# Kernel optimization log

Measured on AMD Instinct MI355X. Metric: run time of the kernel, lower is better.

The kernel has to match this reference:

```python
import jax, jax.numpy as jnp
import numpy as np

# dims matching input_specs / init_kwargs
S_BATCH, T_BATCH, NUM, DIM, H, W = 4, 4, 8, 512, 32, 32
K = 64              # self.k, number of kmeans clusters
KMEANS_ITERS = 10   # fixed Lloyd iterations (stand-in for kmeans-to-convergence)


def _kmeans(points):
    """Euclidean Lloyd kmeans. points: [n, d] -> centers [K, d].
    Deterministic init: first K points. Empty clusters keep old center."""
    centers0 = points[:K]
    sq_p = jnp.sum(points * points, axis=1)  # [n]

    def step(centers, _):
        # squared euclidean distance [n, K]
        d2 = sq_p[:, None] + jnp.sum(centers * centers, axis=1)[None, :] \
             - 2.0 * points @ centers.T
        assign = jnp.argmin(d2, axis=1)                      # [n]
        onehot = jax.nn.one_hot(assign, K, dtype=points.dtype)  # [n, K]
        counts = onehot.sum(axis=0)                          # [K]
        sums = onehot.T @ points                             # [K, d]
        new = jnp.where(counts[:, None] > 0,
                        sums / jnp.maximum(counts, 1.0)[:, None],
                        centers)
        return new, None

    centers, _ = jax.lax.scan(step, centers0, None, length=KMEANS_ITERS)
    return centers


def setup_inputs() -> dict:
    key = jax.random.key(0)
    k1, k2, k3, k4 = jax.random.split(key, 4)
    return {
        "source_feat": jax.random.normal(k1, (S_BATCH, NUM, DIM, H, W), dtype=jnp.float32),
        "target_feat": jax.random.normal(k2, (T_BATCH, NUM, DIM, H, W), dtype=jnp.float32),
        "source_label": jax.random.randint(k3, (S_BATCH,), 0, 10),
        "target_label": jax.random.randint(k4, (T_BATCH,), 0, 10),
    }


def reference(source_feat, target_feat, source_label, target_label):
    sb, num, dim, h, w = source_feat.shape
    tb = target_feat.shape[0]

    # view each map as (h*w, dim) point cloud, kmeans per (batch, num)
    s_pts = source_feat.reshape(sb, num, dim, h * w).transpose(0, 1, 3, 2)
    t_pts = target_feat.reshape(tb, num, dim, h * w).transpose(0, 1, 3, 2)
    km = jax.vmap(jax.vmap(_kmeans))
    cs = km(s_pts).transpose(1, 0, 2, 3)  # [num, sb, K, dim]
    ct = km(t_pts).transpose(1, 0, 2, 3)  # [num, tb, K, dim]

    # mat_dist for every (num, i, j) pair of center sets: [num, sb, tb, K, K]
    sq_s = jnp.sum(cs * cs, axis=-1)  # [num, sb, K]
    sq_t = jnp.sum(ct * ct, axis=-1)  # [num, tb, K]
    dots = jnp.einsum('nikd,njld->nijkl', cs, ct)
    dist = jnp.sqrt(jnp.maximum(
        sq_s[:, :, None, :, None] + sq_t[:, None, :, None, :] - 2.0 * dots, 0.0))
    y = jnp.argmin(dist, axis=-1)  # [num, sb, tb, K] nearest target center per source center

    # gather matched target centers; replicate source centers over j (torch append order: i, j, k)
    ct_b = jnp.broadcast_to(ct[:, None], (num, sb, tb, K, dim))
    t_mat = jnp.take_along_axis(ct_b, y[..., None], axis=3)            # [num, sb, tb, K, dim]
    s_mat = jnp.broadcast_to(cs[:, :, None], (num, sb, tb, K, dim))

    N = sb * tb * K
    s_mat = s_mat.reshape(num, N, dim)
    t_mat = t_mat.reshape(num, N, dim)

    # trans_mat[k] = s_mat.T @ pinv(t_mat.T)   -> [num, dim, dim]
    pinv_t = jnp.linalg.pinv(t_mat.transpose(0, 2, 1))  # pinv([dim, N]) -> [num, N, dim]
    trans_mat = jnp.einsum('nkd,nke->nde', s_mat, pinv_t)
    return trans_mat
```

## Files before the change

### kernel.cpp

```cpp
#include <hip/hip_runtime.h>

typedef unsigned int u32;
typedef unsigned long long u64;

#define NPTS  1024
#define DIMD  512
#define KCL   64
#define KMIT  10

constexpr size_t O_CTG  = 0;
constexpr size_t O_SUMS = O_CTG  + 64ull*512*64;
constexpr size_t O_CNT  = O_SUMS + 64ull*64*512;
constexpr size_t O_SQC  = O_CNT  + 64ull*64;
constexpr size_t O_SQP  = O_SQC  + 64ull*64;
constexpr size_t O_ASG  = O_SQP  + 64ull*1024;
constexpr size_t O_CTN  = O_ASG  + 64ull*1024;
constexpr size_t O_Y    = O_CTN  + 8ull*256*512;
constexpr size_t O_CNT2 = O_Y    + 8ull*4*4*64;
constexpr size_t O_BM   = O_CNT2 + 8ull*256;
constexpr size_t O_G    = O_BM   + 8ull*256*512;
constexpr size_t O_LT   = O_G    + 8ull*256*256;
constexpr size_t O_YB   = O_LT   + 8ull*256*256;
constexpr size_t O_ZB   = O_YB   + 8ull*256*512;
constexpr size_t O_PTST = O_ZB   + 8ull*256*512;

constexpr size_t O_PS0 = O_SUMS;
constexpr size_t O_PS1 = O_CTN;
static_assert(O_PS1 + 64ull*64*512 <= O_G, "PS1 overlay must fit before O_G");

constexpr size_t O_BEST = O_G;

constexpr size_t O_CS = O_SUMS;
constexpr size_t O_W  = O_YB;
constexpr size_t O_WT = O_YB + 8ull*4*64*64;

__device__ __forceinline__ const float* run_base(const float* s, const float* t, int run){
    const float* b = (run < 32) ? s : t;
    return b + (size_t)(run & 31) * (DIMD * NPTS);
}
__device__ __forceinline__ u64 dpack(float d2, int c){
    u32 u = __float_as_uint(d2);
    u = (u & 0x80000000u) ? ~u : (u | 0x80000000u);
    return ((u64)u << 32) | (u32)c;
}
__device__ __forceinline__ float rdlane(float v, int l){
    return __uint_as_float(__builtin_amdgcn_readlane(__float_as_uint(v), l));
}

__global__ __launch_bounds__(256) void k_init(const float* __restrict__ src, const float* __restrict__ tgt,
                                              float* __restrict__ ws){
    int bx = blockIdx.x; int run = bx >> 2, q = bx & 3;
    int tid = threadIdx.x;
    const float* base = run_base(src, tgt, run);
    int p = q*256 + tid;
    float acc = 0.f;
    for (int d = 0; d < DIMD; ++d){
        float v = base[(size_t)d*NPTS + p];
        acc = fmaf(v, v, acc);
    }
    ws[O_SQP + run*NPTS + p] = acc;
    if (q == 0){
        if (tid < KCL) ws[O_SQC + run*KCL + tid] = acc;
        if (tid < KCL) ((int*)(ws + O_CNT))[run*KCL + tid] = 0;
        for (int idx = tid; idx < DIMD*KCL; idx += 256){
            int d = idx >> 6, c = idx & 63;
            ws[O_CTG + (size_t)run*DIMD*KCL + idx] = base[(size_t)d*NPTS + c];
        }
    }
}

__global__ __launch_bounds__(256) void k_ptsT(const float* __restrict__ src, const float* __restrict__ tgt,
                                              float* __restrict__ ws){
    int bx = blockIdx.x; int dt = bx & 7, pt = (bx >> 3) & 15, run = bx >> 7;
    int tid = threadIdx.x, lane = tid & 63, r4 = tid >> 6;
    const float* base = run_base(src, tgt, run);
    __shared__ float t[64*65];
    for (int pass = 0; pass < 16; ++pass){
        int r = pass*4 + r4;
        t[r*65 + lane] = base[(size_t)(dt*64 + r)*NPTS + pt*64 + lane];
    }
    __syncthreads();
    for (int pass = 0; pass < 16; ++pass){
        int p = pass*4 + r4;
        ws[O_PTST + ((size_t)run*NPTS + pt*64 + p)*DIMD + dt*64 + lane] = t[lane*65 + p];
    }
}

__global__ __launch_bounds__(256, 4) void k_assign(const float* __restrict__ src, const float* __restrict__ tgt,
                                                   const float* __restrict__ ctr, const float* __restrict__ sqc,
                                                   const float* __restrict__ sqp,
                                                   u64* __restrict__ bestg){
    int bxx = blockIdx.x;
    int cb  = (bxx >> 3) & 1;
    int w   = ((bxx >> 4) << 3) | (bxx & 7);
    int run = w >> 3, qt = w & 7;
    int tid = threadIdx.x, lane = tid & 63;
    int g = __builtin_amdgcn_readfirstlane(tid >> 6);
    int c0 = cb*32 + g*8;
    const float* base = run_base(src, tgt, run);
    const float* cg = ctr + (size_t)run*DIMD*KCL + c0;
    int p0 = qt*128 + 2*lane;
    float acc[2][8] = {};
    __shared__ u64 red[4][128];

#define LOADP(P, DB) { \
    _Pragma("unroll") \
    for (int u = 0; u < 8; ++u) \
        P[u] = *(const float2*)&base[(size_t)((DB)*8 + u)*NPTS + p0]; }

#define COMPUTE(P, DB) { \
    _Pragma("unroll") \
    for (int u = 0; u < 8; ++u){ \
        const float4* cp = (const float4*)(cg + (size_t)((DB)*8 + u)*KCL); \
        float4 c0v = cp[0], c1v = cp[1]; \
        float cv[8] = {c0v.x,c0v.y,c0v.z,c0v.w, c1v.x,c1v.y,c1v.z,c1v.w}; \
        _Pragma("unroll") \
        for (int cl = 0; cl < 8; ++cl){ \
            acc[0][cl] = fmaf(P[u].x, cv[cl], acc[0][cl]); \
            acc[1][cl] = fmaf(P[u].y, cv[cl], acc[1][cl]); \
        } \
    } }

    float2 pa[8], pb[8];
    LOADP(pa, 0);
    for (int db = 0; db < 64; db += 2){
        if (db + 1 < 64) LOADP(pb, db + 1);
        COMPUTE(pa, db);
        if (db + 2 < 64) LOADP(pa, db + 2);
        COMPUTE(pb, db + 1);
    }
#undef LOADP
#undef COMPUTE

    const float* sqcg = sqc + run*KCL + c0;
    float sq[8];
    #pragma unroll
    for (int q = 0; q < 8; ++q) sq[q] = sqcg[q];
    float2 sq2 = *(const float2*)&sqp[run*NPTS + p0];
    #pragma unroll
    for (int s = 0; s < 2; ++s){
        float sqpv = s ? sq2.y : sq2.x;
        u64 best = dpack(sqpv + sq[0] - 2.f*acc[s][0], c0);
        #pragma unroll
        for (int cl = 1; cl < 8; ++cl){
            u64 k2 = dpack(sqpv + sq[cl] - 2.f*acc[s][cl], c0 + cl);
            best = (k2 < best) ? k2 : best;
        }
        red[g][2*lane + s] = best;
    }
    __syncthreads();
    if (tid < 128){
        u64 b = red[0][tid];
        #pragma unroll
        for (int g2 = 1; g2 < 4; ++g2){ u64 k2 = red[g2][tid]; b = (k2 < b) ? k2 : b; }
        bestg[(((size_t)(run*8 + qt)*128 + tid) << 1) + cb] = b;
    }
}

__global__ __launch_bounds__(256) void k_sums(float* __restrict__ ws){
    int bx = blockIdx.x; int pg = bx & 1, dh = (bx >> 1) & 1, run = bx >> 2;
    int tid = threadIdx.x;
    __shared__ float sm[KCL*256];
    __shared__ int a[512];
    const u64* bestg = (const u64*)(ws + O_BEST);
    int* cnt = (int*)(ws + O_CNT);
    for (int idx = tid; idx < 512; idx += 256){
        int p = pg*512 + idx;
        int qt = p >> 7, t = p & 127;
        const u64* bp = bestg + (((size_t)(run*8 + qt)*128 + t) << 1);
        u64 x = bp[0], y = bp[1];
        u64 m = (y < x) ? y : x;
        int c = (int)(m & 0xffffffffu);
        a[idx] = c;
        if (dh == 0) atomicAdd(&cnt[run*KCL + c], 1);
    }
    for (int idx = tid; idx < KCL*256; idx += 256) sm[idx] = 0.f;
    __syncthreads();
    const float* pT = ws + O_PTST + ((size_t)run*NPTS + pg*512)*DIMD + dh*256 + tid;
    for (int p = 0; p < 512; p += 4){
        float v0 = pT[(size_t)(p+0)*DIMD], v1 = pT[(size_t)(p+1)*DIMD];
        float v2 = pT[(size_t)(p+2)*DIMD], v3 = pT[(size_t)(p+3)*DIMD];
        sm[a[p+0]*256 + tid] += v0;
        sm[a[p+1]*256 + tid] += v1;
        sm[a[p+2]*256 + tid] += v2;
        sm[a[p+3]*256 + tid] += v3;
    }
    __syncthreads();
    size_t psx = pg ? O_PS1 : O_PS0;
    for (int c = 0; c < KCL; ++c)
        ws[psx + ((size_t)run*KCL + c)*DIMD + dh*256 + tid] = sm[c*256 + tid];
}

__global__ __launch_bounds__(256) void k_newc(float* __restrict__ ws){
    int run = blockIdx.x, tid = threadIdx.x;
    __shared__ float sm2[KCL*65];
    __shared__ int cl[KCL];
    int* cnt = (int*)(ws + O_CNT);
    if (tid < KCL) cl[tid] = cnt[run*KCL + tid];
    __syncthreads();
    if (tid < KCL) cnt[run*KCL + tid] = 0;
    float sqa = 0.f;
    for (int dc = 0; dc < 8; ++dc){
        for (int idx = tid; idx < KCL*64; idx += 256){
            int c = idx >> 6, dl = idx & 63;
            size_t o = ((size_t)run*KCL + c)*DIMD + dc*64 + dl;
            sm2[c*65 + dl] = ws[O_PS0 + o] + ws[O_PS1 + o];
        }
        __syncthreads();
        for (int idx = tid; idx < KCL*64; idx += 256){
            int dl = idx >> 6, c = idx & 63, d = dc*64 + dl;
            size_t gi = O_CTG + (size_t)run*DIMD*KCL + d*KCL + c;
            float old = ws[gi];
            int cc = cl[c];
            float nv = (cc > 0) ? sm2[c*65 + dl] / (float)cc : old;
            ws[gi] = nv;
            sm2[c*65 + dl] = nv;
        }
        __syncthreads();
        if (tid < KCL){
            for (int dl = 0; dl < 64; ++dl){ float v = sm2[tid*65 + dl]; sqa = fmaf(v, v, sqa); }
        }
        __syncthreads();
    }
    if (tid < KCL) ws[O_SQC + run*KCL + tid] = sqa;
}

__global__ __launch_bounds__(256) void k_ctn(float* __restrict__ ws){
    int bx = blockIdx.x; int dc = bx & 7, jj = (bx >> 3) & 3, n = (bx >> 5) & 7, st = bx >> 8;
    int run = st ? (jj*8 + n) : (32 + jj*8 + n);
    int tid = threadIdx.x, lane = tid & 63, r4 = tid >> 6;
    __shared__ float t[64*65];
    for (int pass = 0; pass < 16; ++pass){
        int r = pass*4 + r4;
        t[r*65 + lane] = ws[O_CTG + (size_t)run*DIMD*KCL + (dc*64 + r)*KCL + lane];
    }
    __syncthreads();
    size_t dstbase = st ? (O_CS  + ((size_t)(n*4 + jj)*64)*DIMD)
                        : (O_CTN + ((size_t)n*256 + jj*64)*DIMD);
    for (int pass = 0; pass < 16; ++pass){
        int l = pass*4 + r4;
        ws[dstbase + (size_t)l*DIMD + dc*64 + lane] = t[lane*65 + l];
    }
}

__global__ __launch_bounds__(256) void k_map(float* __restrict__ ws){
    int bx = blockIdx.x; int j = bx & 3, i = (bx >> 2) & 3, n = bx >> 4;
    int run_s = i*8 + n, run_t = 32 + j*8 + n;
    int tid = threadIdx.x, lane = tid & 63;
    int g = __builtin_amdgcn_readfirstlane(tid >> 6);
    const float* cgs = ws + O_CTG + (size_t)run_s*DIMD*KCL + lane;
    const float* cgt = ws + O_CTG + (size_t)run_t*DIMD*KCL + g*16;
    float acc[16] = {};
    for (int d = 0; d < DIMD; ++d){
        float csv = cgs[d*KCL];
        const float4* cp = (const float4*)(cgt + d*KCL);
        float4 c0=cp[0], c1=cp[1], c2=cp[2], c3=cp[3];
        float cv[16] = {c0.x,c0.y,c0.z,c0.w, c1.x,c1.y,c1.z,c1.w,
                        c2.x,c2.y,c2.z,c2.w, c3.x,c3.y,c3.z,c3.w};
        #pragma unroll
        for (int cl = 0; cl < 16; ++cl) acc[cl] = fmaf(csv, cv[cl], acc[cl]);
    }
    float sqs = ws[O_SQC + run_s*KCL + lane];
    const float* sqtp = ws + O_SQC + run_t*KCL + g*16;
    u64 best = dpack(sqs + sqtp[0] - 2.f*acc[0], g*16);
    #pragma unroll
    for (int cl = 1; cl < 16; ++cl){
        u64 k2 = dpack(sqs + sqtp[cl] - 2.f*acc[cl], g*16 + cl);
        best = (k2 < best) ? k2 : best;
    }
    __shared__ u64 red[4][64];
    red[g][lane] = best;
    __syncthreads();
    if (tid < 64){
        u64 b = red[0][tid];
        #pragma unroll
        for (int g2 = 1; g2 < 4; ++g2){ u64 k2 = red[g2][tid]; b = (k2 < b) ? k2 : b; }
        int l = (int)(b & 0xffffffffu);
        int* yv   = (int*)(ws + O_Y);
        int* cnt2 = (int*)(ws + O_CNT2);
        yv[((n*4 + i)*4 + j)*64 + tid] = l;
        atomicAdd(&cnt2[n*256 + j*64 + l], 1);
    }
}

__global__ __launch_bounds__(256) void k_bmat(float* __restrict__ ws){
    int bx = blockIdx.x; int dh = bx & 1, j = (bx >> 1) & 3, n = bx >> 3;
    int tid = threadIdx.x;
    __shared__ float Bacc[KCL*256];
    __shared__ int yl[256];
    __shared__ int c2[KCL];
    const int* yv   = (const int*)(ws + O_Y);
    const int* cnt2 = (const int*)(ws + O_CNT2);
    { int i = tid >> 6, k = tid & 63; yl[tid] = yv[((n*4 + i)*4 + j)*64 + k]; }
    if (tid < KCL) c2[tid] = cnt2[n*256 + j*64 + tid];
    for (int idx = tid; idx < KCL*256; idx += 256) Bacc[idx] = 0.f;
    __syncthreads();
    const float* cs = ws + O_CS + (size_t)(n*4)*64*DIMD + dh*256 + tid;
    #pragma unroll 4
    for (int s = 0; s < 256; ++s){
        int l = yl[s];
        float v = cs[(size_t)s*DIMD];
        Bacc[l*256 + tid] += v;
    }
    __syncthreads();
    for (int l = 0; l < KCL; ++l){
        int cc = c2[l]; if (cc < 1) cc = 1;
        ws[O_BM + ((size_t)n*256 + j*64 + l)*DIMD + dh*256 + tid] = Bacc[l*256 + tid] / (float)cc;
    }
}

__global__ __launch_bounds__(256) void k_gram(float* __restrict__ ws){
    int bx = blockIdx.x; int cc = bx & 7, n = bx >> 3;
    int tid = threadIdx.x, llane = tid & 63, jlane = tid >> 6;
    int run_t = 32 + jlane*8 + n;
    const float* bbase = ws + O_CTG + (size_t)run_t*DIMD*KCL + llane;
    const float* arow  = ws + O_CTN + (size_t)(n*256 + cc*32)*DIMD;
    float acc[32] = {};
    for (int d = 0; d < DIMD; d += 4){
        float bv0 = bbase[(d+0)*KCL], bv1 = bbase[(d+1)*KCL];
        float bv2 = bbase[(d+2)*KCL], bv3 = bbase[(d+3)*KCL];
        #pragma unroll
        for (int c = 0; c < 32; ++c){
            const float4 av = *(const float4*)&arow[c*DIMD + d];
            acc[c] = fmaf(av.x, bv0, acc[c]);
            acc[c] = fmaf(av.y, bv1, acc[c]);
            acc[c] = fmaf(av.z, bv2, acc[c]);
            acc[c] = fmaf(av.w, bv3, acc[c]);
        }
    }
    const int* cnt2 = (const int*)(ws + O_CNT2);
    bool used_cp = cnt2[n*256 + tid] > 0;
    float* Gp = ws + O_G + (size_t)n*65536;
    #pragma unroll
    for (int c = 0; c < 32; ++c){
        int cg = cc*32 + c;
        bool used_c = cnt2[n*256 + cg] > 0;
        float v = (used_c && used_cp) ? acc[c] : ((cg == tid) ? 1.f : 0.f);
        Gp[(size_t)cg*256 + tid] = v;
    }
}

__global__ __launch_bounds__(256, 1) void k_chol(float* __restrict__ ws){
    int n = blockIdx.x, tid = threadIdx.x;
    int lane = tid & 63, wv = tid >> 6;
    float* Gn  = ws + O_G  + (size_t)n*65536;
    float* LTn = ws + O_LT + (size_t)n*65536;
    __shared__ __align__(16) float Pc[64*200];

    for (int kb = 0; kb < 4; ++kb){
        int c0 = kb*64, r1 = c0 + 64, rem = 256 - r1;
        float dreg[64];
        {
            const float* grow = Gn + (size_t)(c0+lane)*256 + c0;
            #pragma unroll
            for (int j4 = 0; j4 < 16; ++j4){
                float4 v = *(const float4*)&grow[j4*4];
                dreg[j4*4+0]=v.x; dreg[j4*4+1]=v.y; dreg[j4*4+2]=v.z; dreg[j4*4+3]=v.w;
            }
        }
        float preg[64];
        int prow = (wv-1)*64 + lane;
        bool pact = (wv >= 1) && (prow < rem);
        {
            const float* growp = Gn + (size_t)(r1+prow)*256 + c0;
            #pragma unroll
            for (int j4 = 0; j4 < 16; ++j4){
                if (pact){
                    float4 v = *(const float4*)&growp[j4*4];
                    preg[j4*4+0]=v.x; preg[j4*4+1]=v.y; preg[j4*4+2]=v.z; preg[j4*4+3]=v.w;
                } else {
                    preg[j4*4+0]=0.f; preg[j4*4+1]=0.f; preg[j4*4+2]=0.f; preg[j4*4+3]=0.f;
                }
            }
        }
        #pragma unroll
        for (int k = 0; k < 64; ++k){
            float dkk = sqrtf(fmaxf(rdlane(dreg[k], k), 1e-30f));
            float inv = 1.f / dkk;
            dreg[k] = (lane == k) ? dkk : dreg[k]*inv;
            preg[k] *= inv;
            #pragma unroll
            for (int j = k+1; j < 64; ++j){
                float s = rdlane(dreg[k], j);
                dreg[j] = fmaf(-dreg[k], s, dreg[j]);
                preg[j] = fmaf(-preg[k], s, preg[j]);
            }
        }
        if (wv == 0){
            float* grow = Gn + (size_t)(c0+lane)*256 + c0;
            #pragma unroll
            for (int j4 = 0; j4 < 16; ++j4){
                float4 v; v.x=dreg[j4*4+0]; v.y=dreg[j4*4+1]; v.z=dreg[j4*4+2]; v.w=dreg[j4*4+3];
                *(float4*)&grow[j4*4] = v;
            }
        }
        if (pact){
            float* growp = Gn + (size_t)(r1+prow)*256 + c0;
            #pragma unroll
            for (int j4 = 0; j4 < 16; ++j4){
                float4 v; v.x=preg[j4*4+0]; v.y=preg[j4*4+1]; v.z=preg[j4*4+2]; v.w=preg[j4*4+3];
                *(float4*)&growp[j4*4] = v;
            }
            float* ltp = LTn + (size_t)c0*256 + r1 + prow;
            #pragma unroll
            for (int j = 0; j < 64; ++j) ltp[(size_t)j*256] = preg[j];
            #pragma unroll
            for (int j = 0; j < 64; ++j) Pc[j*200 + prow] = preg[j];
        }
        __syncthreads();
        if (rem > 0){
            int nt4 = rem >> 2;
            int ntiles = nt4*(nt4+1)/2;
            for (int t = tid; t < ntiles; t += 256){
                int ti = (int)((sqrtf(8.f*(float)t + 1.f) - 1.f) * 0.5f);
                while ((ti+1)*(ti+2)/2 <= t) ++ti;
                while (ti*(ti+1)/2 > t) --ti;
                int tj = t - ti*(ti+1)/2;
                int i0 = ti*4, j0 = tj*4;
                float acc[4][4] = {};
                for (int k = 0; k < 64; ++k){
                    const float4 pi = *(const float4*)&Pc[k*200 + i0];
                    const float4 pj = *(const float4*)&Pc[k*200 + j0];
                    float pir[4] = {pi.x,pi.y,pi.z,pi.w};
                    float pjr[4] = {pj.x,pj.y,pj.z,pj.w};
                    #pragma unroll
                    for (int r = 0; r < 4; ++r)
                        #pragma unroll
                        for (int s = 0; s < 4; ++s)
                            acc[r][s] = fmaf(pir[r], pjr[s], acc[r][s]);
                }
                #pragma unroll
                for (int r = 0; r < 4; ++r){
                    float* grow = Gn + (size_t)(r1+i0+r)*256 + r1 + j0;
                    #pragma unroll
                    for (int s = 0; s < 4; ++s) grow[s] -= acc[r][s];
                }
            }
        }
        __syncthreads();
    }
}

__global__ __launch_bounds__(256, 1) void k_dinv(float* __restrict__ ws){
    int n = blockIdx.x, tid = threadIdx.x;
    int lane = tid & 63, kb = tid >> 6;
    const float* Gn = ws + O_G + (size_t)n*65536;
    __shared__ __align__(16) float DlT[4][64*65];
    for (int idx = lane; idx < 1024; idx += 64){
        int r = idx >> 4, c4 = idx & 15;
        float4 v = *(const float4*)&Gn[(size_t)(kb*64 + r)*256 + kb*64 + c4*4];
        DlT[kb][(c4*4+0)*65 + r] = v.x;
        DlT[kb][(c4*4+1)*65 + r] = v.y;
        DlT[kb][(c4*4+2)*65 + r] = v.z;
        DlT[kb][(c4*4+3)*65 + r] = v.w;
    }
    __syncthreads();
    float x[64];
    #pragma unroll
    for (int i = 0; i < 64; ++i) x[i] = (i == lane) ? 1.f : 0.f;
    const float* Dk = DlT[kb];
    #pragma unroll
    for (int k = 0; k < 64; ++k){
        float invd = 1.f / Dk[k*65 + k];
        x[k] *= invd;
        #pragma unroll
        for (int i = k+1; i < 64; ++i)
            x[i] = fmaf(-Dk[k*65 + i], x[k], x[i]);
    }
    float* Wg  = ws + O_W  + ((size_t)n*4 + kb)*4096;
    float* WTg = ws + O_WT + ((size_t)n*4 + kb)*4096;
    #pragma unroll
    for (int r = 0; r < 64; ++r) Wg[r*64 + lane] = x[r];
    #pragma unroll
    for (int r4 = 0; r4 < 16; ++r4){
        float4 v; v.x=x[r4*4+0]; v.y=x[r4*4+1]; v.z=x[r4*4+2]; v.w=x[r4*4+3];
        *(float4*)&WTg[lane*64 + r4*4] = v;
    }
}

__global__ __launch_bounds__(256, 1) void k_solve(float* __restrict__ ws){
    int n = blockIdx.x, cg = blockIdx.y;
    int tid = threadIdx.x;
    int tx = tid & 15, ty = tid >> 4;
    const float* Gn  = ws + O_G  + (size_t)n*65536;
    const float* LTn = ws + O_LT + (size_t)n*65536;
    const float* Ct  = ws + O_CTN + (size_t)n*256*DIMD + (size_t)cg*64;
    const float* Wg  = ws + O_W  + (size_t)n*4*4096;
    const float* WTg = ws + O_WT + (size_t)n*4*4096;
    float* Zb = ws + O_ZB + (size_t)n*256*DIMD + (size_t)cg*64;

    __shared__ __align__(16) float YL[4][64*65];
    __shared__ __align__(16) float At[64*65];
    __shared__ __align__(16) float RL[64*65];

    float acc[4][4];
    for (int bi = 0; bi < 4; ++bi){
        #pragma unroll
        for (int a = 0; a < 4; ++a){
            float4 v = *(const float4*)&Ct[(size_t)(bi*64 + ty*4 + a)*DIMD + tx*4];
            acc[a][0]=v.x; acc[a][1]=v.y; acc[a][2]=v.z; acc[a][3]=v.w;
        }
        for (int j = 0; j < bi; ++j){
            __syncthreads();
            for (int idx = tid; idx < 1024; idx += 256){
                int k = idx >> 4, r4 = idx & 15;
                float4 v = *(const float4*)&LTn[(size_t)(j*64 + k)*256 + bi*64 + r4*4];
                *(float4*)&At[k*65 + r4*4] = v;
            }
            __syncthreads();
            const float* Yj = YL[j];
            #pragma unroll 8
            for (int k = 0; k < 64; ++k){
                float4 av = *(const float4*)&At[k*65 + ty*4];
                float4 yv = *(const float4*)&Yj[k*65 + tx*4];
                float ar[4] = {av.x,av.y,av.z,av.w};
                float yr[4] = {yv.x,yv.y,yv.z,yv.w};
                #pragma unroll
                for (int a = 0; a < 4; ++a)
                    #pragma unroll
                    for (int b = 0; b < 4; ++b)
                        acc[a][b] = fmaf(-ar[a], yr[b], acc[a][b]);
            }
        }
        __syncthreads();
        #pragma unroll
        for (int a = 0; a < 4; ++a){
            float4 v; v.x=acc[a][0]; v.y=acc[a][1]; v.z=acc[a][2]; v.w=acc[a][3];
            *(float4*)&RL[(ty*4 + a)*65 + tx*4] = v;
        }
        for (int idx = tid; idx < 1024; idx += 256){
            int k = idx >> 4, r4 = idx & 15;
            float4 v = *(const float4*)&WTg[(size_t)bi*4096 + k*64 + r4*4];
            *(float4*)&At[k*65 + r4*4] = v;
        }
        __syncthreads();
        float out[4][4] = {};
        #pragma unroll 8
        for (int k = 0; k < 64; ++k){
            float4 av = *(const float4*)&At[k*65 + ty*4];
            float4 rv = *(const float4*)&RL[k*65 + tx*4];
            float ar[4] = {av.x,av.y,av.z,av.w};
            float rr[4] = {rv.x,rv.y,rv.z,rv.w};
            #pragma unroll
            for (int a = 0; a < 4; ++a)
                #pragma unroll
                for (int b = 0; b < 4; ++b)
                    out[a][b] = fmaf(ar[a], rr[b], out[a][b]);
        }
        float* Yi = YL[bi];
        #pragma unroll
        for (int a = 0; a < 4; ++a){
            float4 v; v.x=out[a][0]; v.y=out[a][1]; v.z=out[a][2]; v.w=out[a][3];
            *(float4*)&Yi[(ty*4 + a)*65 + tx*4] = v;
        }
    }
    for (int bi = 3; bi >= 0; --bi){
        __syncthreads();
        #pragma unroll
        for (int a = 0; a < 4; ++a){
            float4 v = *(const float4*)&YL[bi][(ty*4 + a)*65 + tx*4];
            acc[a][0]=v.x; acc[a][1]=v.y; acc[a][2]=v.z; acc[a][3]=v.w;
        }
        for (int j = bi+1; j < 4; ++j){
            __syncthreads();
            for (int idx = tid; idx < 1024; idx += 256){
                int k = idx >> 4, r4 = idx & 15;
                float4 v = *(const float4*)&Gn[(size_t)(j*64 + k)*256 + bi*64 + r4*4];
                *(float4*)&At[k*65 + r4*4] = v;
            }
            __syncthreads();
            const float* Zj = YL[j];
            #pragma unroll 8
            for (int k = 0; k < 64; ++k){
                float4 av = *(const float4*)&At[k*65 + ty*4];
                float4 zv = *(const float4*)&Zj[k*65 + tx*4];
                float ar[4] = {av.x,av.y,av.z,av.w};
                float zr[4] = {zv.x,zv.y,zv.z,zv.w};
                #pragma unroll
                for (int a = 0; a < 4; ++a)
                    #pragma unroll
                    for (int b = 0; b < 4; ++b)
                        acc[a][b] = fmaf(-ar[a], zr[b], acc[a][b]);
            }
        }
        __syncthreads();
        #pragma unroll
        for (int a = 0; a < 4; ++a){
            float4 v; v.x=acc[a][0]; v.y=acc[a][1]; v.z=acc[a][2]; v.w=acc[a][3];
            *(float4*)&RL[(ty*4 + a)*65 + tx*4] = v;
        }
        for (int idx = tid; idx < 1024; idx += 256){
            int k = idx >> 4, r4 = idx & 15;
            float4 v = *(const float4*)&Wg[(size_t)bi*4096 + k*64 + r4*4];
            *(float4*)&At[k*65 + r4*4] = v;
        }
        __syncthreads();
        float out[4][4] = {};
        #pragma unroll 8
        for (int k = 0; k < 64; ++k){
            float4 av = *(const float4*)&At[k*65 + ty*4];
            float4 rv = *(const float4*)&RL[k*65 + tx*4];
            float ar[4] = {av.x,av.y,av.z,av.w};
            float rr[4] = {rv.x,rv.y,rv.z,rv.w};
            #pragma unroll
            for (int a = 0; a < 4; ++a)
                #pragma unroll
                for (int b = 0; b < 4; ++b)
                    out[a][b] = fmaf(ar[a], rr[b], out[a][b]);
        }
        float* Zi = YL[bi];
        #pragma unroll
        for (int a = 0; a < 4; ++a){
            float4 v; v.x=out[a][0]; v.y=out[a][1]; v.z=out[a][2]; v.w=out[a][3];
            *(float4*)&Zi[(ty*4 + a)*65 + tx*4] = v;
            *(float4*)&Zb[(size_t)(bi*64 + ty*4 + a)*DIMD + tx*4] = v;
        }
    }
}

__global__ __launch_bounds__(256) void k_gemmE(const float* __restrict__ ws, float* __restrict__ out){
    int bx = blockIdx.x; int et = bx & 7, dt = (bx >> 3) & 7, n = bx >> 6;
    int tid = threadIdx.x;
    __shared__ float Bl[256*64];
    __shared__ float Zl[256*64];
    const float* Bm = ws + O_BM + (size_t)n*256*DIMD;
    const float* Zb = ws + O_ZB + (size_t)n*256*DIMD;
    for (int idx = tid; idx < 16384; idx += 256){
        int c = idx >> 6, dd = idx & 63;
        Bl[idx] = Bm[(size_t)c*DIMD + dt*64 + dd];
        Zl[idx] = Zb[(size_t)c*DIMD + et*64 + dd];
    }
    __syncthreads();
    int td = tid & 15, te = tid >> 4;
    float acc[4][4] = {};
    for (int c = 0; c < 256; ++c){
        float4 bv = *(const float4*)&Bl[c*64 + td*4];
        float4 zv = *(const float4*)&Zl[c*64 + te*4];
        float b4[4] = {bv.x, bv.y, bv.z, bv.w};
        float z4[4] = {zv.x, zv.y, zv.z, zv.w};
        #pragma unroll
        for (int r = 0; r < 4; ++r)
            #pragma unroll
            for (int s = 0; s < 4; ++s) acc[r][s] = fmaf(b4[r], z4[s], acc[r][s]);
    }
    float* ob = out + (size_t)n*262144 + (size_t)(dt*64 + td*4)*DIMD + et*64 + te*4;
    #pragma unroll
    for (int r = 0; r < 4; ++r){
        float4 o; o.x = acc[r][0]; o.y = acc[r][1]; o.z = acc[r][2]; o.w = acc[r][3];
        *(float4*)&ob[(size_t)r*DIMD] = o;
    }
}

extern "C" void kernel_launch(void* const* d_in, const int* in_sizes, int n_in,
                              void* d_out, int out_size, void* d_ws, size_t ws_size,
                              hipStream_t stream){
    const float* src = (const float*)d_in[0];
    const float* tgt = (const float*)d_in[1];
    float* ws  = (float*)d_ws;
    float* out = (float*)d_out;

    k_init<<<256, 256, 0, stream>>>(src, tgt, ws);
    k_ptsT<<<8192, 256, 0, stream>>>(src, tgt, ws);

    for (int it = 0; it < KMIT; ++it){
        k_assign<<<1024, 256, 0, stream>>>(src, tgt,
                                           ws + O_CTG, ws + O_SQC, ws + O_SQP,
                                           (u64*)(ws + O_BEST));
        k_sums<<<256, 256, 0, stream>>>(ws);
        k_newc<<<64, 256, 0, stream>>>(ws);
    }

    hipMemsetAsync((char*)d_ws + O_CNT2*4, 0, 8*256*4, stream);
    k_ctn<<<512, 256, 0, stream>>>(ws);
    k_map<<<128, 256, 0, stream>>>(ws);
    k_bmat<<<64, 256, 0, stream>>>(ws);
    k_gram<<<64, 256, 0, stream>>>(ws);
    k_chol<<<8, 256, 0, stream>>>(ws);
    k_dinv<<<8, 256, 0, stream>>>(ws);
    k_solve<<<dim3(8, 8), 256, 0, stream>>>(ws);
    k_gemmE<<<512, 256, 0, stream>>>(ws, out);
}
```

Measured before the change: 2.413 ms.

## Split blocked Cholesky into panel and trailing-update kernels; deepen assign prefetch

The single-block-per-matrix Cholesky is split into a per-panel factor kernel and a separate trailing-update kernel launched across 64 blocks per step. The trailing update now reads the panel from global memory instead of shared memory. The aim is to spread the serial Cholesky work across many more CUs, at the cost of extra launches and global reads. Separately, the k_assign loop now loads and computes 16 dimensions per stage instead of 8, which raises register pressure.

```diff
diff --git a/kernel.cpp b/kernel.cpp
--- a/kernel.cpp
+++ b/kernel.cpp
@@ -103,15 +103,15 @@
     float acc[2][8] = {};
     __shared__ u64 red[4][128];
 
-#define LOADP(P, DB) { \
+#define LOADP(P, B) { \
     _Pragma("unroll") \
-    for (int u = 0; u < 8; ++u) \
-        P[u] = *(const float2*)&base[(size_t)((DB)*8 + u)*NPTS + p0]; }
-
-#define COMPUTE(P, DB) { \
+    for (int u = 0; u < 16; ++u) \
+        P[u] = *(const float2*)&base[(size_t)((B)*16 + u)*NPTS + p0]; }
+
+#define COMPUTE(P, B) { \
     _Pragma("unroll") \
-    for (int u = 0; u < 8; ++u){ \
-        const float4* cp = (const float4*)(cg + (size_t)((DB)*8 + u)*KCL); \
+    for (int u = 0; u < 16; ++u){ \
+        const float4* cp = (const float4*)(cg + (size_t)((B)*16 + u)*KCL); \
         float4 c0v = cp[0], c1v = cp[1]; \
         float cv[8] = {c0v.x,c0v.y,c0v.z,c0v.w, c1v.x,c1v.y,c1v.z,c1v.w}; \
         _Pragma("unroll") \
@@ -121,13 +121,13 @@
         } \
     } }
 
-    float2 pa[8], pb[8];
+    float2 pa[16], pb[16];
     LOADP(pa, 0);
-    for (int db = 0; db < 64; db += 2){
-        if (db + 1 < 64) LOADP(pb, db + 1);
-        COMPUTE(pa, db);
-        if (db + 2 < 64) LOADP(pa, db + 2);
-        COMPUTE(pb, db + 1);
+    for (int b = 0; b < 32; b += 2){
+        if (b + 1 < 32) LOADP(pb, b + 1);
+        COMPUTE(pa, b);
+        if (b + 2 < 32) LOADP(pa, b + 2);
+        COMPUTE(pb, b + 1);
     }
 #undef LOADP
 #undef COMPUTE
@@ -340,104 +340,115 @@
     }
 }
 
-__global__ __launch_bounds__(256, 1) void k_chol(float* __restrict__ ws){
+__global__ __launch_bounds__(256, 1) void k_cholp(float* __restrict__ ws, int kb){
     int n = blockIdx.x, tid = threadIdx.x;
     int lane = tid & 63, wv = tid >> 6;
     float* Gn  = ws + O_G  + (size_t)n*65536;
     float* LTn = ws + O_LT + (size_t)n*65536;
-    __shared__ __align__(16) float Pc[64*200];
-
-    for (int kb = 0; kb < 4; ++kb){
-        int c0 = kb*64, r1 = c0 + 64, rem = 256 - r1;
-        float dreg[64];
-        {
-            const float* grow = Gn + (size_t)(c0+lane)*256 + c0;
+    int c0 = kb*64, r1 = c0 + 64, rem = 256 - r1;
+
+    float dreg[64];
+    {
+        const float* grow = Gn + (size_t)(c0+lane)*256 + c0;
+        #pragma unroll
+        for (int j4 = 0; j4 < 16; ++j4){
+            float4 v = *(const float4*)&grow[j4*4];
+            dreg[j4*4+0]=v.x; dreg[j4*4+1]=v.y; dreg[j4*4+2]=v.z; dreg[j4*4+3]=v.w;
+        }
+    }
+    float preg[64];
+    int prow = (wv-1)*64 + lane;
+    bool pact = (wv >= 1) && (prow < rem);
+    {
+        const float* growp = Gn + (size_t)(r1+prow)*256 + c0;
+        #pragma unroll
+        for (int j4 = 0; j4 < 16; ++j4){
+            if (pact){
+                float4 v = *(const float4*)&growp[j4*4];
+                preg[j4*4+0]=v.x; preg[j4*4+1]=v.y; preg[j4*4+2]=v.z; preg[j4*4+3]=v.w;
+            } else {
+                preg[j4*4+0]=0.f; preg[j4*4+1]=0.f; preg[j4*4+2]=0.f; preg[j4*4+3]=0.f;
+            }
+        }
+    }
+    #pragma unroll
+    for (int k = 0; k < 64; ++k){
+        float dkk = sqrtf(fmaxf(rdlane(dreg[k], k), 1e-30f));
+        float inv = 1.f / dkk;
+        dreg[k] = (lane == k) ? dkk : dreg[k]*inv;
+        preg[k] *= inv;
+        #pragma unroll
+        for (int j = k+1; j < 64; ++j){
+            float s = rdlane(dreg[k], j);
+            dreg[j] = fmaf(-dreg[k], s, dreg[j]);
+            preg[j] = fmaf(-preg[k], s, preg[j]);
+        }
+    }
+    if (wv == 0){
+        float* grow = Gn + (size_t)(c0+lane)*256 + c0;
+        #pragma unroll
+        for (int j4 = 0; j4 < 16; ++j4){
+            float4 v; v.x=dreg[j4*4+0]; v.y=dreg[j4*4+1]; v.z=dreg[j4*4+2]; v.w=dreg[j4*4+3];
+            *(float4*)&grow[j4*4] = v;
+        }
+    }
+    if (pact){
+        float* growp = Gn + (size_t)(r1+prow)*256 + c0;
+        #pragma unroll
+        for (int j4 = 0; j4 < 16; ++j4){
+            float4 v; v.x=preg[j4*4+0]; v.y=preg[j4*4+1]; v.z=preg[j4*4+2]; v.w=preg[j4*4+3];
+            *(float4*)&growp[j4*4] = v;
+        }
+        float* ltp = LTn + (size_t)c0*256 + r1 + prow;
+        #pragma unroll
+        for (int j = 0; j < 64; ++j) ltp[(size_t)j*256] = preg[j];
+    }
+}
+
+__global__ __launch_bounds__(256) void k_trail(float* __restrict__ ws, int kb){
+    int n = blockIdx.y;
+    int c0 = kb*64, r1 = c0 + 64, rem = 256 - r1;
+    int nt4 = rem >> 2;
+    int ntiles = nt4*(nt4+1)/2;
+    float* Gn = ws + O_G + (size_t)n*65536;
+    for (int t = blockIdx.x*256 + threadIdx.x; t < ntiles; t += gridDim.x*256){
+        int ti = (int)((sqrtf(8.f*(float)t + 1.f) - 1.f) * 0.5f);
+        while ((ti+1)*(ti+2)/2 <= t) ++ti;
+        while (ti*(ti+1)/2 > t) --ti;
+        int tj = t - ti*(ti+1)/2;
+        int i0 = ti*4, j0 = tj*4;
+        const float* Li = Gn + (size_t)(r1+i0)*256 + c0;
+        const float* Lj = Gn + (size_t)(r1+j0)*256 + c0;
+        float acc[4][4] = {};
+        for (int k = 0; k < 64; k += 4){
+            float4 ar4[4], br4[4];
             #pragma unroll
-            for (int j4 = 0; j4 < 16; ++j4){
-                float4 v = *(const float4*)&grow[j4*4];
-                dreg[j4*4+0]=v.x; dreg[j4*4+1]=v.y; dreg[j4*4+2]=v.z; dreg[j4*4+3]=v.w;
+            for (int r = 0; r < 4; ++r) ar4[r] = *(const float4*)&Li[(size_t)r*256 + k];
+            #pragma unroll
+            for (int s = 0; s < 4; ++s) br4[s] = *(const float4*)&Lj[(size_t)s*256 + k];
+            #pragma unroll
+            for (int q = 0; q < 4; ++q){
+                float aq[4] = { q==0?ar4[0].x:q==1?ar4[0].y:q==2?ar4[0].z:ar4[0].w,
+                                q==0?ar4[1].x:q==1?ar4[1].y:q==2?ar4[1].z:ar4[1].w,
+                                q==0?ar4[2].x:q==1?ar4[2].y:q==2?ar4[2].z:ar4[2].w,
+                                q==0?ar4[3].x:q==1?ar4[3].y:q==2?ar4[3].z:ar4[3].w };
+                float bq[4] = { q==0?br4[0].x:q==1?br4[0].y:q==2?br4[0].z:br4[0].w,
+                                q==0?br4[1].x:q==1?br4[1].y:q==2?br4[1].z:br4[1].w,
+                                q==0?br4[2].x:q==1?br4[2].y:q==2?br4[2].z:br4[2].w,
+                                q==0?br4[3].x:q==1?br4[3].y:q==2?br4[3].z:br4[3].w };
+                #pragma unroll
+                for (int r = 0; r < 4; ++r)
+                    #pragma unroll
+                    for (int s = 0; s < 4; ++s)
+                        acc[r][s] = fmaf(aq[r], bq[s], acc[r][s]);
             }
         }
-        float preg[64];
-        int prow = (wv-1)*64 + lane;
-        bool pact = (wv >= 1) && (prow < rem);
-        {
-            const float* growp = Gn + (size_t)(r1+prow)*256 + c0;
+        #pragma unroll
+        for (int r = 0; r < 4; ++r){
+            float* grow = Gn + (size_t)(r1+i0+r)*256 + r1 + j0;
             #pragma unroll
-            for (int j4 = 0; j4 < 16; ++j4){
-                if (pact){
-                    float4 v = *(const float4*)&growp[j4*4];
-                    preg[j4*4+0]=v.x; preg[j4*4+1]=v.y; preg[j4*4+2]=v.z; preg[j4*4+3]=v.w;
-                } else {
-                    preg[j4*4+0]=0.f; preg[j4*4+1]=0.f; preg[j4*4+2]=0.f; preg[j4*4+3]=0.f;
-                }
-            }
-        }
-        #pragma unroll
-        for (int k = 0; k < 64; ++k){
-            float dkk = sqrtf(fmaxf(rdlane(dreg[k], k), 1e-30f));
-            float inv = 1.f / dkk;
-            dreg[k] = (lane == k) ? dkk : dreg[k]*inv;
-            preg[k] *= inv;
-            #pragma unroll
-            for (int j = k+1; j < 64; ++j){
-                float s = rdlane(dreg[k], j);
-                dreg[j] = fmaf(-dreg[k], s, dreg[j]);
-                preg[j] = fmaf(-preg[k], s, preg[j]);
-            }
-        }
-        if (wv == 0){
-            float* grow = Gn + (size_t)(c0+lane)*256 + c0;
-            #pragma unroll
-            for (int j4 = 0; j4 < 16; ++j4){
-                float4 v; v.x=dreg[j4*4+0]; v.y=dreg[j4*4+1]; v.z=dreg[j4*4+2]; v.w=dreg[j4*4+3];
-                *(float4*)&grow[j4*4] = v;
-            }
-        }
-        if (pact){
-            float* growp = Gn + (size_t)(r1+prow)*256 + c0;
-            #pragma unroll
-            for (int j4 = 0; j4 < 16; ++j4){
-                float4 v; v.x=preg[j4*4+0]; v.y=preg[j4*4+1]; v.z=preg[j4*4+2]; v.w=preg[j4*4+3];
-                *(float4*)&growp[j4*4] = v;
-            }
-            float* ltp = LTn + (size_t)c0*256 + r1 + prow;
-            #pragma unroll
-            for (int j = 0; j < 64; ++j) ltp[(size_t)j*256] = preg[j];
-            #pragma unroll
-            for (int j = 0; j < 64; ++j) Pc[j*200 + prow] = preg[j];
-        }
-        __syncthreads();
-        if (rem > 0){
-            int nt4 = rem >> 2;
-            int ntiles = nt4*(nt4+1)/2;
-            for (int t = tid; t < ntiles; t += 256){
-                int ti = (int)((sqrtf(8.f*(float)t + 1.f) - 1.f) * 0.5f);
-                while ((ti+1)*(ti+2)/2 <= t) ++ti;
-                while (ti*(ti+1)/2 > t) --ti;
-                int tj = t - ti*(ti+1)/2;
-                int i0 = ti*4, j0 = tj*4;
-                float acc[4][4] = {};
-                for (int k = 0; k < 64; ++k){
-                    const float4 pi = *(const float4*)&Pc[k*200 + i0];
-                    const float4 pj = *(const float4*)&Pc[k*200 + j0];
-                    float pir[4] = {pi.x,pi.y,pi.z,pi.w};
-                    float pjr[4] = {pj.x,pj.y,pj.z,pj.w};
-                    #pragma unroll
-                    for (int r = 0; r < 4; ++r)
-                        #pragma unroll
-                        for (int s = 0; s < 4; ++s)
-                            acc[r][s] = fmaf(pir[r], pjr[s], acc[r][s]);
-                }
-                #pragma unroll
-                for (int r = 0; r < 4; ++r){
-                    float* grow = Gn + (size_t)(r1+i0+r)*256 + r1 + j0;
-                    #pragma unroll
-                    for (int s = 0; s < 4; ++s) grow[s] -= acc[r][s];
-                }
-            }
-        }
-        __syncthreads();
+            for (int s = 0; s < 4; ++s) grow[s] -= acc[r][s];
+        }
     }
 }
 
@@ -675,7 +686,10 @@
     k_map<<<128, 256, 0, stream>>>(ws);
     k_bmat<<<64, 256, 0, stream>>>(ws);
     k_gram<<<64, 256, 0, stream>>>(ws);
-    k_chol<<<8, 256, 0, stream>>>(ws);
+    for (int kb = 0; kb < 4; ++kb){
+        k_cholp<<<8, 256, 0, stream>>>(ws, kb);
+        if (kb < 3) k_trail<<<dim3(8, 8), 256, 0, stream>>>(ws, kb);
+    }
     k_dinv<<<8, 256, 0, stream>>>(ws);
     k_solve<<<dim3(8, 8), 256, 0, stream>>>(ws);
     k_gemmE<<<512, 256, 0, stream>>>(ws, out);
```

After: 2.598 ms. 1.08x slower.
